# Optimization experiments

Measured on AMD Instinct MI355X. Metric: run time of the kernel, lower is better.

Reference implementation:

```python
import jax, jax.numpy as jnp
import numpy as np

Z, Y, X = 32, 480, 480          # sparse voxel grid (LiDAR-scale)
N = 200_000                     # active voxels
C_IN, C_OUT = 64, 64
EPS = 1e-5


def _subm_conv(f, nbr, w):
    """Submanifold sparse conv as gather-matmul-accumulate.
    f: [N, Cin]; nbr: [N, K] neighbor row ids, pad index == N for missing;
    w: [K, Cin, Cout]."""
    f_pad = jnp.concatenate([f, jnp.zeros((1, f.shape[1]), f.dtype)], axis=0)
    g = f_pad[nbr]                       # [N, K, Cin] gathered neighbor features
    return jnp.einsum('nkc,kco->no', g, w)


def _bn(x, gamma, beta):
    # BatchNorm1d in training mode: batch stats over the N dimension
    m = x.mean(axis=0)
    v = x.var(axis=0)
    return (x - m) * jax.lax.rsqrt(v + EPS) * gamma + beta


def setup_inputs() -> dict:
    rng = np.random.default_rng(0)
    ids = rng.choice(Z * Y * X, size=N, replace=False)
    lookup = np.full(Z * Y * X, -1, dtype=np.int64)
    lookup[ids] = np.arange(N)
    z = ids // (Y * X)
    y = (ids // X) % Y
    x = ids % X

    def nbr_table(offsets):
        cols = []
        for dz, dy, dx in offsets:
            zz, yy, xx = z + dz, y + dy, x + dx
            ok = (zz >= 0) & (zz < Z) & (yy >= 0) & (yy < Y) & (xx >= 0) & (xx < X)
            lin = np.clip((zz * Y + yy) * X + xx, 0, Z * Y * X - 1)
            idx = np.where(ok, lookup[lin], -1)
            cols.append(np.where(idx >= 0, idx, N))   # pad index N -> zero row
        return jnp.asarray(np.stack(cols, axis=1).astype(np.int32))

    off13 = [(0, dy, dx) for dy in (-1, 0, 1) for dx in (-1, 0, 1)]  # kernel (1,3,3)
    off31 = [(dz, 0, dx) for dz in (-1, 0, 1) for dx in (-1, 0, 1)]  # kernel (3,1,3)

    key = jax.random.key(0)
    ks = jax.random.split(key, 5)
    s = 0.05
    ones = jnp.ones((C_OUT,), jnp.float32)
    zeros = jnp.zeros((C_OUT,), jnp.float32)
    return {
        'features': jax.random.normal(ks[0], (N, C_IN), jnp.float32),
        'w1':   jax.random.normal(ks[1], (9, C_IN, C_OUT), jnp.float32) * s,
        'w1_2': jax.random.normal(ks[2], (9, C_OUT, C_OUT), jnp.float32) * s,
        'w2':   jax.random.normal(ks[3], (9, C_IN, C_OUT), jnp.float32) * s,
        'w3':   jax.random.normal(ks[4], (9, C_OUT, C_OUT), jnp.float32) * s,
        'g0': ones, 'b0': zeros, 'g0_2': ones, 'b0_2': zeros,
        'g1': ones, 'b1': zeros, 'g2': ones, 'b2': zeros,
        'nbr13': nbr_table(off13),
        'nbr31': nbr_table(off31),
    }


def reference(features, w1, w1_2, w2, w3, g0, b0, g0_2, b0_2, g1, b1, g2, b2,
              nbr13, nbr31):
    # shortcut branch: conv1x3 -> LeakyReLU -> BN -> conv3x1 -> LeakyReLU -> BN
    sc = _subm_conv(features, nbr13, w1)
    sc = _bn(jax.nn.leaky_relu(sc), g0, b0)
    sc = _subm_conv(sc, nbr31, w1_2)
    sc = _bn(jax.nn.leaky_relu(sc), g0_2, b0_2)
    # main branch: conv3x1 -> LeakyReLU -> BN -> conv1x3 -> LeakyReLU -> BN
    r = _subm_conv(features, nbr31, w2)
    r = _bn(jax.nn.leaky_relu(r), g1, b1)
    r = _subm_conv(r, nbr13, w3)
    r = _bn(jax.nn.leaky_relu(r), g2, b2)
    return r + sc
```

## Files before the change

kernel.cpp:

```cpp
#include <hip/hip_runtime.h>

#define NVOX 200000
#define TM 128
#define NBLK 1563
#define NREP 32
#define STG 4224

typedef unsigned short u16;
typedef unsigned int u32;
typedef __bf16 bf16x8 __attribute__((ext_vector_type(8)));
typedef float f32x16 __attribute__((ext_vector_type(16)));

__device__ __forceinline__ float bf2f(u16 h) { return __uint_as_float(((u32)h) << 16); }
__device__ __forceinline__ u16 f2bf(float x) {
  u32 u = __float_as_uint(x);
  u32 r = u + 0x7fffu + ((u >> 16) & 1u);
  return (u16)(r >> 16);
}
__device__ __forceinline__ uint4 cvt8(uint4 a, uint4 b) {
  const float* fa = (const float*)&a;
  const float* fb = (const float*)&b;
  uint4 r;
  u16* q = (u16*)&r;
#pragma unroll
  for (int j = 0; j < 4; ++j) { q[j] = f2bf(fa[j]); q[4 + j] = f2bf(fb[j]); }
  return r;
}

template <int PHASE>
__global__ __launch_bounds__(256, 4)
void conv_fused(const u16* __restrict__ inA, const u16* __restrict__ inB,
                const int* __restrict__ nbrA, const int* __restrict__ nbrB,
                const u16* __restrict__ wfA, const u16* __restrict__ wfB,
                const u16* __restrict__ zrow,
                void* yA, void* yB, float* __restrict__ stA, float* __restrict__ stB) {
  __shared__ __align__(16) float fb4[64 * 68];
  __shared__ float sred[4][128];

  const int tid = threadIdx.x;
  const int bid = blockIdx.x;
  const bool hB = (bid >= NBLK);
  const int blk = hB ? bid - NBLK : bid;
  const u16* f = hB ? inB : inA;
  const int* nbr = hB ? nbrB : nbrA;
  const u16* wf = hB ? wfB : wfA;
  float* st = hB ? stB : stA;

  const int wv = tid >> 6;
  const int lane = tid & 63;
  const int lrow = lane & 31;
  const int lq = lane >> 5;
  const int base = blk * TM;
  const int gr = base + wv * 32 + lrow;

  int ids[9];
#pragma unroll
  for (int j = 0; j < 9; ++j) ids[j] = (gr < NVOX) ? nbr[gr * 9 + j] : NVOX;

  f32x16 acc0 = {0.f, 0.f, 0.f, 0.f, 0.f, 0.f, 0.f, 0.f,
                 0.f, 0.f, 0.f, 0.f, 0.f, 0.f, 0.f, 0.f};
  f32x16 acc1 = acc0;
  constexpr bool FOLDED = (PHASE == 1);
  constexpr int KSTRIDE = FOLDED ? 5120 : 4096;

  uint4 bufA[4], bufB[4];

  auto lda = [&](uint4 (&d)[4], int k) {
    const u16* p = (ids[k] < NVOX) ? (f + (size_t)ids[k] * 64) : zrow;
    p += lq * 8;
#pragma unroll
    for (int i = 0; i < 4; ++i) d[i] = *(const uint4*)(p + i * 16);
  };

  auto mma = [&](const uint4 (&s)[4], int k) {
    const u16* wb = wf + k * KSTRIDE;
#pragma unroll
    for (int ksi = 0; ksi < 4; ++ksi) {
      bf16x8 a = __builtin_bit_cast(bf16x8, s[ksi]);
      bf16x8 b0 = __builtin_bit_cast(bf16x8, *(const uint4*)(wb + (ksi * 2) * 512 + lane * 8));
      bf16x8 b1 = __builtin_bit_cast(bf16x8, *(const uint4*)(wb + (ksi * 2 + 1) * 512 + lane * 8));
      acc0 = __builtin_amdgcn_mfma_f32_32x32x16_bf16(a, b0, acc0, 0, 0, 0);
      acc1 = __builtin_amdgcn_mfma_f32_32x32x16_bf16(a, b1, acc1, 0, 0, 0);
    }
    if constexpr (FOLDED) {
      uint4 a4 = make_uint4(0u, 0u, 0u, 0u);
      if (lq == 0 && ids[k] < NVOX) ((u16*)&a4)[0] = 0x3F80u;
      bf16x8 a = __builtin_bit_cast(bf16x8, a4);
      bf16x8 b0 = __builtin_bit_cast(bf16x8, *(const uint4*)(wb + 8 * 512 + lane * 8));
      bf16x8 b1 = __builtin_bit_cast(bf16x8, *(const uint4*)(wb + 9 * 512 + lane * 8));
      acc0 = __builtin_amdgcn_mfma_f32_32x32x16_bf16(a, b0, acc0, 0, 0, 0);
      acc1 = __builtin_amdgcn_mfma_f32_32x32x16_bf16(a, b1, acc1, 0, 0, 0);
    }
  };

  lda(bufA, 0); lda(bufB, 1);
  mma(bufA, 0);
  lda(bufA, 2); mma(bufB, 1);
  lda(bufB, 3); mma(bufA, 2);
  lda(bufA, 4); mma(bufB, 3);
  lda(bufB, 5); mma(bufA, 4);
  lda(bufA, 6); mma(bufB, 5);
  lda(bufB, 7); mma(bufA, 6);
  lda(bufA, 8); mma(bufB, 7);
  mma(bufA, 8);

  const int cc0 = lrow, cc1 = 32 + lrow;
  float s0 = 0.f, q0 = 0.f, s1 = 0.f, q1 = 0.f;
  float vout[2][16];
#pragma unroll
  for (int r = 0; r < 16; ++r) {
    float v = acc0[r]; v = v > 0.f ? v : 0.01f * v;
    s0 += v; q0 += v * v; vout[0][r] = v;
    float w = acc1[r]; w = w > 0.f ? w : 0.01f * w;
    s1 += w; q1 += w * w; vout[1][r] = w;
  }
  s0 += __shfl_xor(s0, 32); q0 += __shfl_xor(q0, 32);
  s1 += __shfl_xor(s1, 32); q1 += __shfl_xor(q1, 32);
  if (lq == 0) {
    sred[wv][lrow] = s0; sred[wv][32 + lrow] = s1;
    sred[wv][64 + lrow] = q0; sred[wv][96 + lrow] = q1;
  }

  const bool f32out = (PHASE == 1) && !hB;
  const int trow = tid >> 3, cp = tid & 7;
  u16* bb = (u16*)fb4;
#pragma unroll
  for (int h = 0; h < 2; ++h) {
    __syncthreads();
    if ((wv >> 1) == h) {
      const int lr = 32 * (wv & 1);
#pragma unroll
      for (int r = 0; r < 16; ++r) {
        int rowD = lr + (r & 3) + 8 * (r >> 2) + 4 * lq;
        if (f32out) {
          fb4[rowD * 68 + cc0] = vout[0][r];
          fb4[rowD * 68 + cc1] = vout[1][r];
        } else {
          bb[rowD * 72 + cc0] = f2bf(vout[0][r]);
          bb[rowD * 72 + cc1] = f2bf(vout[1][r]);
        }
      }
    }
    __syncthreads();
    if (f32out) {
      float* y = (float*)yA;
#pragma unroll
      for (int it = 0; it < 2; ++it) {
        int r = it * 32 + trow, row = base + 64 * h + r;
        if (row < NVOX) {
          *(float4*)(y + (size_t)row * 64 + cp * 8) = *(const float4*)(fb4 + r * 68 + cp * 8);
          *(float4*)(y + (size_t)row * 64 + cp * 8 + 4) = *(const float4*)(fb4 + r * 68 + cp * 8 + 4);
        }
      }
    } else {
      u16* y = (u16*)(hB ? yB : yA);
#pragma unroll
      for (int it = 0; it < 2; ++it) {
        int r = it * 32 + trow, row = base + 64 * h + r;
        if (row < NVOX)
          *(uint4*)(y + (size_t)row * 64 + cp * 8) = *(const uint4*)(bb + r * 72 + cp * 8);
      }
    }
  }
  if (tid < 128) {
    int which = tid >> 6, c = tid & 63;
    float v = sred[0][which * 64 + c] + sred[1][which * 64 + c] +
              sred[2][which * 64 + c] + sred[3][which * 64 + c];
    atomicAdd(&st[(bid & (NREP - 1)) * 128 + which * 64 + c], v);
  }
}

template <bool IN_F32, bool FOLDED, int MODE>
__global__ __launch_bounds__(256, 4)
void conv_k(const void* __restrict__ fv, const int* __restrict__ nbr,
            const u16* __restrict__ wf, void* yv, float* __restrict__ st,
            float* io, const float* __restrict__ affD,
            const float* __restrict__ affB) {
  __shared__ __align__(16) float fb[128 * 68];
  __shared__ float sred[4][128];

  const int tid = threadIdx.x;
  const int wv = tid >> 6;
  const int lane = tid & 63;
  const int lrow = lane & 31;
  const int lq = lane >> 5;
  const int base = blockIdx.x * TM;
  const int gr = base + wv * 32 + lrow;

  int ids[9];
#pragma unroll
  for (int j = 0; j < 9; ++j) ids[j] = (gr < NVOX) ? nbr[gr * 9 + j] : NVOX;

  f32x16 acc0 = {0.f, 0.f, 0.f, 0.f, 0.f, 0.f, 0.f, 0.f,
                 0.f, 0.f, 0.f, 0.f, 0.f, 0.f, 0.f, 0.f};
  f32x16 acc1 = acc0;
  constexpr int KSTRIDE = FOLDED ? 5120 : 4096;

#pragma unroll
  for (int k = 0; k < 9; ++k) {
    if (k != 4) {
      if (__ballot(ids[k] < NVOX) == 0ull) continue;
    }
    const int id = ids[k];
    const bool ok = id < NVOX;
    uint4 af[4];
    if constexpr (IN_F32) {
      const float* p = (const float*)fv + (size_t)id * 64 + lq * 8;
#pragma unroll
      for (int ksi = 0; ksi < 4; ++ksi) {
        uint4 v0 = make_uint4(0u, 0u, 0u, 0u), v1 = v0;
        if (ok) { v0 = *(const uint4*)(p + ksi * 16); v1 = *(const uint4*)(p + ksi * 16 + 4); }
        af[ksi] = cvt8(v0, v1);
      }
    } else {
      const u16* p = (const u16*)fv + (size_t)id * 64 + lq * 8;
#pragma unroll
      for (int ksi = 0; ksi < 4; ++ksi) {
        uint4 v = make_uint4(0u, 0u, 0u, 0u);
        if (ok) v = *(const uint4*)(p + ksi * 16);
        af[ksi] = v;
      }
    }
    const u16* wb = wf + k * KSTRIDE;
#pragma unroll
    for (int ksi = 0; ksi < 4; ++ksi) {
      bf16x8 a = __builtin_bit_cast(bf16x8, af[ksi]);
      bf16x8 b0 = __builtin_bit_cast(bf16x8, *(const uint4*)(wb + (ksi * 2) * 512 + lane * 8));
      bf16x8 b1 = __builtin_bit_cast(bf16x8, *(const uint4*)(wb + (ksi * 2 + 1) * 512 + lane * 8));
      acc0 = __builtin_amdgcn_mfma_f32_32x32x16_bf16(a, b0, acc0, 0, 0, 0);
      acc1 = __builtin_amdgcn_mfma_f32_32x32x16_bf16(a, b1, acc1, 0, 0, 0);
    }
    if constexpr (FOLDED) {
      uint4 a4 = make_uint4(0u, 0u, 0u, 0u);
      if (lq == 0 && ok) ((u16*)&a4)[0] = 0x3F80u;
      bf16x8 a = __builtin_bit_cast(bf16x8, a4);
      bf16x8 b0 = __builtin_bit_cast(bf16x8, *(const uint4*)(wb + 8 * 512 + lane * 8));
      bf16x8 b1 = __builtin_bit_cast(bf16x8, *(const uint4*)(wb + 9 * 512 + lane * 8));
      acc0 = __builtin_amdgcn_mfma_f32_32x32x16_bf16(a, b0, acc0, 0, 0, 0);
      acc1 = __builtin_amdgcn_mfma_f32_32x32x16_bf16(a, b1, acc1, 0, 0, 0);
    }
  }

  const int cc0 = lrow, cc1 = 32 + lrow;
  float aD0 = 0.f, aD1 = 0.f, hD0 = 0.f, hD1 = 0.f;
  if constexpr (MODE == 2) {
    aD0 = affD[cc0]; hD0 = affD[64 + cc0];
    aD1 = affD[cc1]; hD1 = affD[64 + cc1];
  }
  float s0 = 0.f, q0 = 0.f, s1 = 0.f, q1 = 0.f;
  float vout[2][16];
#pragma unroll
  for (int r = 0; r < 16; ++r) {
    float v = acc0[r]; v = v > 0.f ? v : 0.01f * v;
    s0 += v; q0 += v * v; vout[0][r] = v;
    float w = acc1[r]; w = w > 0.f ? w : 0.01f * w;
    s1 += w; q1 += w * w; vout[1][r] = w;
  }
  if constexpr (MODE != 2) {
    s0 += __shfl_xor(s0, 32); q0 += __shfl_xor(q0, 32);
    s1 += __shfl_xor(s1, 32); q1 += __shfl_xor(q1, 32);
    if (lq == 0) {
      sred[wv][lrow] = s0; sred[wv][32 + lrow] = s1;
      sred[wv][64 + lrow] = q0; sred[wv][96 + lrow] = q1;
    }
  }
  if constexpr (MODE == 0) {
    u16* bb = (u16*)fb;
#pragma unroll
    for (int r = 0; r < 16; ++r) {
      int rowD = 32 * wv + (r & 3) + 8 * (r >> 2) + 4 * lq;
      bb[rowD * 72 + cc0] = f2bf(vout[0][r]);
      bb[rowD * 72 + cc1] = f2bf(vout[1][r]);
    }
  } else if constexpr (MODE == 2 || MODE == 3) {
#pragma unroll
    for (int r = 0; r < 16; ++r) {
      int rowD = 32 * wv + (r & 3) + 8 * (r >> 2) + 4 * lq;
      float v0 = vout[0][r], v1 = vout[1][r];
      if constexpr (MODE == 2) { v0 = fmaf(v0, aD0, hD0); v1 = fmaf(v1, aD1, hD1); }
      fb[rowD * 68 + cc0] = v0;
      fb[rowD * 68 + cc1] = v1;
    }
  }
  __syncthreads();

  const int trow = tid >> 3, cp = tid & 7;
  if constexpr (MODE == 0) {
    u16* y = (u16*)yv;
    const u16* bb = (const u16*)fb;
#pragma unroll
    for (int it = 0; it < 4; ++it) {
      int r = it * 32 + trow, row = base + r;
      if (row < NVOX)
        *(uint4*)(y + (size_t)row * 64 + cp * 8) = *(const uint4*)(bb + r * 72 + cp * 8);
    }
  }
  if constexpr (MODE == 3) {
    float* y = (float*)yv;
#pragma unroll
    for (int it = 0; it < 4; ++it) {
      int r = it * 32 + trow, row = base + r;
      if (row < NVOX) {
        *(float4*)(y + (size_t)row * 64 + cp * 8) = *(const float4*)(fb + r * 68 + cp * 8);
        *(float4*)(y + (size_t)row * 64 + cp * 8 + 4) = *(const float4*)(fb + r * 68 + cp * 8 + 4);
      }
    }
  }
  if constexpr (MODE == 2) {
    float* y = (float*)yv;
#pragma unroll
    for (int it = 0; it < 4; ++it) {
      int r = it * 32 + trow, row = base + r;
      if (row < NVOX) {
        float t[8], p[8], o[8];
        *(float4*)&t[0] = *(const float4*)(fb + r * 68 + cp * 8);
        *(float4*)&t[4] = *(const float4*)(fb + r * 68 + cp * 8 + 4);
        *(float4*)&p[0] = *(const float4*)(io + (size_t)row * 64 + cp * 8);
        *(float4*)&p[4] = *(const float4*)(io + (size_t)row * 64 + cp * 8 + 4);
#pragma unroll
        for (int j = 0; j < 8; ++j) {
          int c = cp * 8 + j;
          o[j] = t[j] + fmaf(p[j], affB[c], affB[64 + c]);
        }
        *(float4*)(y + (size_t)row * 64 + cp * 8) = *(const float4*)&o[0];
        *(float4*)(y + (size_t)row * 64 + cp * 8 + 4) = *(const float4*)&o[4];
      }
    }
  }
  if constexpr (MODE != 2) {
    if (tid < 128) {
      int which = tid >> 6, c = tid & 63;
      float v = sred[0][which * 64 + c] + sred[1][which * 64 + c] +
                sred[2][which * 64 + c] + sred[3][which * 64 + c];
      atomicAdd(&st[(blockIdx.x & (NREP - 1)) * 128 + which * 64 + c], v);
    }
  }
}

__global__ void prep_all(const float* __restrict__ feat, const float* __restrict__ w1,
                         const float* __restrict__ w2, u16* __restrict__ wf,
                         u16* __restrict__ F, float* __restrict__ st,
                         u16* __restrict__ zr, int cvt_blocks) {
  const int bid = blockIdx.x, tid = threadIdx.x;
  if (bid < cvt_blocks) {
    int i8 = (bid * 256 + tid) * 8;
    if (i8 < NVOX * 64) {
      uint4 a = *(const uint4*)(feat + i8);
      uint4 b = *(const uint4*)(feat + i8 + 4);
      *(uint4*)(F + i8) = cvt8(a, b);
    }
    return;
  }
  int rb = bid - cvt_blocks;
  if (rb < 288) {
    int e = rb * 256 + tid;
    int slot = e / 36864, r = e % 36864;
    int k = r >> 12, rr = r & 4095;
    int frag = rr >> 9, lane = (rr >> 3) & 63, j = rr & 7;
    int ks = frag >> 1, ct = frag & 1;
    int cin = ks * 16 + (lane >> 5) * 8 + j;
    int cout = ct * 32 + (lane & 31);
    const float* src = slot ? w2 : w1;
    wf[e] = f2bf(src[k * 4096 + cin * 64 + cout]);
    return;
  }
  for (int i = tid; i < 4 * STG; i += 256) st[i] = 0.f;
  if (tid < 32) ((u32*)zr)[tid] = 0u;
}

__device__ __forceinline__ void bn_from_replicas(const float* stp, const float* g,
                                                 const float* b, int c,
                                                 float* sc, float* sh) {
  float s = 0.f, q = 0.f;
#pragma unroll
  for (int r = 0; r < NREP; ++r) {
    s += stp[r * 128 + c];
    q += stp[r * 128 + 64 + c];
  }
  const float invn = 1.0f / (float)NVOX;
  float mean = s * invn;
  float var = q * invn - mean * mean;
  float sca = g[c] * rsqrtf(var + 1e-5f);
  *sc = sca;
  *sh = b[c] - mean * sca;
}

__global__ void wscale2(const float* __restrict__ wA, float* __restrict__ stpA,
                        const float* __restrict__ gA, const float* __restrict__ bA,
                        u16* __restrict__ dA,
                        const float* __restrict__ wB, float* __restrict__ stpB,
                        const float* __restrict__ gB, const float* __restrict__ bB,
                        u16* __restrict__ dB) {
  __shared__ float sc[64], sh[64];
  const int tid = threadIdx.x;
  const bool hB = (blockIdx.x >= 180);
  const float* wraw = hB ? wB : wA;
  float* stp = hB ? stpB : stpA;
  const float* g = hB ? gB : gA;
  const float* b = hB ? bB : bA;
  u16* dst = hB ? dB : dA;
  const int blk = hB ? blockIdx.x - 180 : blockIdx.x;
  if (tid < 64) {
    float a, h;
    bn_from_replicas(stp, g, b, tid, &a, &h);
    sc[tid] = a; sh[tid] = h;
    if (blk == 0) { stp[NREP * 128 + tid] = a; stp[NREP * 128 + 64 + tid] = h; }
  }
  __syncthreads();
  int e = blk * 256 + tid;
  int k = e / 5120, r = e % 5120;
  int frag = r >> 9, lane = (r >> 3) & 63, j = r & 7;
  int ks = frag >> 1, ct = frag & 1;
  int cout = ct * 32 + (lane & 31);
  u16 val = 0;
  if (ks < 4) {
    int cin = ks * 16 + (lane >> 5) * 8 + j;
    val = f2bf(sc[cin] * wraw[k * 4096 + cin * 64 + cout]);
  } else if (((lane >> 5) == 0) && j == 0) {
    float acc = 0.f;
    for (int c = 0; c < 64; ++c) acc += sh[c] * wraw[k * 4096 + c * 64 + cout];
    val = f2bf(acc);
  }
  dst[e] = val;
}

__global__ void finalize2(float* __restrict__ stA, const float* __restrict__ gA,
                          const float* __restrict__ bA, float* __restrict__ stB,
                          const float* __restrict__ gB, const float* __restrict__ bB) {
  int t = threadIdx.x;
  float* stp = (t < 64) ? stA : stB;
  const float* g = (t < 64) ? gA : gB;
  const float* b = (t < 64) ? bA : bB;
  int c = t & 63;
  if (t < 128) {
    float a, h;
    bn_from_replicas(stp, g, b, c, &a, &h);
    stp[NREP * 128 + c] = a;
    stp[NREP * 128 + 64 + c] = h;
  }
}

__global__ void final_add(const u16* __restrict__ y3, float* io,
                          const float* __restrict__ affB, const float* __restrict__ affD) {
  int i8 = (blockIdx.x * 256 + threadIdx.x) * 8;
  if (i8 < NVOX * 64) {
    float a[8];
    *(float4*)&a[0] = *(const float4*)(io + i8);
    *(float4*)&a[4] = *(const float4*)(io + i8 + 4);
    uint4 vd = *(const uint4*)(y3 + i8);
    const u16* pd = (const u16*)&vd;
    int cb = i8 & 63;
    float o[8];
#pragma unroll
    for (int j = 0; j < 8; ++j) {
      int c = cb + j;
      o[j] = fmaf(a[j], affB[c], affB[64 + c]) + fmaf(bf2f(pd[j]), affD[c], affD[64 + c]);
    }
    *(float4*)(io + i8) = *(const float4*)&o[0];
    *(float4*)(io + i8 + 4) = *(const float4*)&o[4];
  }
}

extern "C" void kernel_launch(void* const* d_in, const int* in_sizes, int n_in,
                              void* d_out, int out_size, void* d_ws, size_t ws_size,
                              hipStream_t stream) {
  const float* feat = (const float*)d_in[0];
  const float* w1 = (const float*)d_in[1];
  const float* w1_2 = (const float*)d_in[2];
  const float* w2 = (const float*)d_in[3];
  const float* w3 = (const float*)d_in[4];
  const float* g0 = (const float*)d_in[5];
  const float* b0 = (const float*)d_in[6];
  const float* g0_2 = (const float*)d_in[7];
  const float* b0_2 = (const float*)d_in[8];
  const float* g1 = (const float*)d_in[9];
  const float* b1 = (const float*)d_in[10];
  const float* g2 = (const float*)d_in[11];
  const float* b2 = (const float*)d_in[12];
  const int* nbr13 = (const int*)d_in[13];
  const int* nbr31 = (const int*)d_in[14];
  float* out = (float*)d_out;

  char* ws = (char*)d_ws;
  float* st = (float*)ws;
  u16* wf = (u16*)(ws + 67584);
  u16* s0 = wf;
  u16* s1 = wf + 36864;
  u16* s2 = wf + 73728;
  u16* s3 = wf + 119808;
  u16* zr = (u16*)(ws + 399360);
  u16* F = (u16*)(ws + 399488);
  u16* A1 = F + (size_t)NVOX * 64;
  u16* A2 = A1 + (size_t)NVOX * 64;
  const size_t base_sz = 399488;
  const size_t need_fused = base_sz + 3ull * NVOX * 64 * 2;
  const size_t need_serial = base_sz + 2ull * NVOX * 64 * 2;

  float* st0 = st, *st1 = st + STG, *st2 = st + 2 * STG, *st3 = st + 3 * STG;

  if (ws_size >= need_fused) {
    prep_all<<<6539, 256, 0, stream>>>(feat, w1, w2, wf, F, st, zr, 6250);
    conv_fused<0><<<2 * NBLK, 256, 0, stream>>>(F, F, nbr13, nbr31, s0, s1, zr,
                                                A1, A2, st0, st2);
    wscale2<<<360, 256, 0, stream>>>(w1_2, st0, g0, b0, s2, w3, st2, g1, b1, s3);
    conv_fused<1><<<2 * NBLK, 256, 0, stream>>>(A1, A2, nbr31, nbr13, s2, s3, zr,
                                                out, F, st1, st3);
    finalize2<<<1, 128, 0, stream>>>(st1, g0_2, b0_2, st3, g2, b2);
    final_add<<<6250, 256, 0, stream>>>(F, out, st1 + NREP * 128, st3 + NREP * 128);
  } else if (ws_size >= need_serial) {
    prep_all<<<6539, 256, 0, stream>>>(feat, w1, w2, wf, F, st, zr, 6250);
    conv_k<false, false, 0><<<NBLK, 256, 0, stream>>>(F, nbr13, s0, A1, st0, nullptr, nullptr, nullptr);
    wscale2<<<180, 256, 0, stream>>>(w1_2, st0, g0, b0, s2, w3, st2, g1, b1, s3);
    conv_k<false, true, 3><<<NBLK, 256, 0, stream>>>(A1, nbr31, s2, out, st1, nullptr, nullptr, nullptr);
    conv_k<false, false, 0><<<NBLK, 256, 0, stream>>>(F, nbr31, s1, A1, st2, nullptr, nullptr, nullptr);
    wscale2<<<360, 256, 0, stream>>>(w1_2, st0, g0, b0, s2, w3, st2, g1, b1, s3);
    conv_k<false, true, 0><<<NBLK, 256, 0, stream>>>(A1, nbr13, s3, F, st3, nullptr, nullptr, nullptr);
    finalize2<<<1, 128, 0, stream>>>(st1, g0_2, b0_2, st3, g2, b2);
    final_add<<<6250, 256, 0, stream>>>(F, out, st1 + NREP * 128, st3 + NREP * 128);
  } else {
    u16* Az = F;
    prep_all<<<289, 256, 0, stream>>>(feat, w1, w2, wf, nullptr, st, zr, 0);
    conv_k<true, false, 0><<<NBLK, 256, 0, stream>>>(feat, nbr13, s0, Az, st0, nullptr, nullptr, nullptr);
    wscale2<<<180, 256, 0, stream>>>(w1_2, st0, g0, b0, s2, w3, st2, g1, b1, s3);
    conv_k<false, true, 3><<<NBLK, 256, 0, stream>>>(Az, nbr31, s2, out, st1, nullptr, nullptr, nullptr);
    finalize2<<<1, 128, 0, stream>>>(st1, g0_2, b0_2, st3, g2, b2);
    conv_k<true, false, 0><<<NBLK, 256, 0, stream>>>(feat, nbr31, s1, Az, st2, nullptr, nullptr, nullptr);
    wscale2<<<360, 256, 0, stream>>>(w1_2, st0, g0, b0, s2, w3, st2, g1, b1, s3);
    conv_k<false, true, 1><<<NBLK, 256, 0, stream>>>(Az, nbr13, s3, nullptr, st3, nullptr, nullptr, nullptr);
    finalize2<<<1, 128, 0, stream>>>(st1, g0_2, b0_2, st3, g2, b2);
    conv_k<false, true, 2><<<NBLK, 256, 0, stream>>>(Az, nbr13, s3, out, nullptr, out,
                                                     st3 + NREP * 128, st1 + NREP * 128);
  }
}
```

Measured before the change: 286.5 us.

## Process three row groups per wave with register-held weights and skip empty neighbors

Each wave now handles 96 rows in three 32-row groups, so every per-offset weight fragment is loaded into registers once and reused across three row groups. Neighbor ids are prefetched one offset ahead, and gathers plus MFMAs are skipped when no lane in a group has a valid neighbor for that offset. The LDS-staged coalesced store epilogue is replaced by direct scattered per-element global stores, and the grid shrinks to a third with launch bounds lowered to 2 blocks per SM. The aim is to cut repeated weight loads and wasted gather/MMA work, at the cost of higher register pressure, lower occupancy and uncoalesced output writes.

```diff
diff --git a/kernel.cpp b/kernel.cpp
--- a/kernel.cpp
+++ b/kernel.cpp
@@ -3,6 +3,7 @@
 #define NVOX 200000
 #define TM 128
 #define NBLK 1563
+#define NBLK3 521
 #define NREP 32
 #define STG 4224
 
@@ -28,19 +29,18 @@
 }
 
 template <int PHASE>
-__global__ __launch_bounds__(256, 4)
+__global__ __launch_bounds__(256, 2)
 void conv_fused(const u16* __restrict__ inA, const u16* __restrict__ inB,
                 const int* __restrict__ nbrA, const int* __restrict__ nbrB,
                 const u16* __restrict__ wfA, const u16* __restrict__ wfB,
                 const u16* __restrict__ zrow,
                 void* yA, void* yB, float* __restrict__ stA, float* __restrict__ stB) {
-  __shared__ __align__(16) float fb4[64 * 68];
   __shared__ float sred[4][128];
 
   const int tid = threadIdx.x;
   const int bid = blockIdx.x;
-  const bool hB = (bid >= NBLK);
-  const int blk = hB ? bid - NBLK : bid;
+  const bool hB = (bid >= NBLK3);
+  const int blk = hB ? bid - NBLK3 : bid;
   const u16* f = hB ? inB : inA;
   const int* nbr = hB ? nbrB : nbrA;
   const u16* wf = hB ? wfB : wfA;
@@ -50,118 +50,113 @@
   const int lane = tid & 63;
   const int lrow = lane & 31;
   const int lq = lane >> 5;
-  const int base = blk * TM;
-  const int gr = base + wv * 32 + lrow;
-
-  int ids[9];
-#pragma unroll
-  for (int j = 0; j < 9; ++j) ids[j] = (gr < NVOX) ? nbr[gr * 9 + j] : NVOX;
-
-  f32x16 acc0 = {0.f, 0.f, 0.f, 0.f, 0.f, 0.f, 0.f, 0.f,
-                 0.f, 0.f, 0.f, 0.f, 0.f, 0.f, 0.f, 0.f};
-  f32x16 acc1 = acc0;
+  const int wbase = blk * 384 + wv * 96;
+  const int gr0 = wbase + lrow;
+  const int gr1 = gr0 + 32;
+  const int gr2 = gr0 + 64;
+
   constexpr bool FOLDED = (PHASE == 1);
   constexpr int KSTRIDE = FOLDED ? 5120 : 4096;
 
-  uint4 bufA[4], bufB[4];
-
-  auto lda = [&](uint4 (&d)[4], int k) {
-    const u16* p = (ids[k] < NVOX) ? (f + (size_t)ids[k] * 64) : zrow;
-    p += lq * 8;
-#pragma unroll
-    for (int i = 0; i < 4; ++i) d[i] = *(const uint4*)(p + i * 16);
+  f32x16 zz = {0.f, 0.f, 0.f, 0.f, 0.f, 0.f, 0.f, 0.f,
+               0.f, 0.f, 0.f, 0.f, 0.f, 0.f, 0.f, 0.f};
+  f32x16 a00 = zz, a01 = zz, a10 = zz, a11 = zz, a20 = zz, a21 = zz;
+
+  int ic0 = (gr0 < NVOX) ? nbr[gr0 * 9] : NVOX;
+  int ic1 = (gr1 < NVOX) ? nbr[gr1 * 9] : NVOX;
+  int ic2 = (gr2 < NVOX) ? nbr[gr2 * 9] : NVOX;
+
+  uint4 X[4], Y[4];
+
+  for (int k = 0; k < 9; ++k) {
+    const u16* wb = wf + k * KSTRIDE;
+    bf16x8 wreg[8];
+#pragma unroll
+    for (int fi = 0; fi < 8; ++fi)
+      wreg[fi] = __builtin_bit_cast(bf16x8, *(const uint4*)(wb + fi * 512 + lane * 8));
+    bf16x8 wrb0, wrb1;
+    if constexpr (FOLDED) {
+      wrb0 = __builtin_bit_cast(bf16x8, *(const uint4*)(wb + 8 * 512 + lane * 8));
+      wrb1 = __builtin_bit_cast(bf16x8, *(const uint4*)(wb + 9 * 512 + lane * 8));
+    }
+    int in0 = NVOX, in1 = NVOX, in2 = NVOX;
+    if (k < 8) {
+      in0 = (gr0 < NVOX) ? nbr[gr0 * 9 + k + 1] : NVOX;
+      in1 = (gr1 < NVOX) ? nbr[gr1 * 9 + k + 1] : NVOX;
+      in2 = (gr2 < NVOX) ? nbr[gr2 * 9 + k + 1] : NVOX;
+    }
+
+    const bool l0 = (k == 4) || (__ballot(ic0 < NVOX) != 0ull);
+    const bool l1 = (k == 4) || (__ballot(ic1 < NVOX) != 0ull);
+    const bool l2 = (k == 4) || (__ballot(ic2 < NVOX) != 0ull);
+
+    auto G = [&](uint4 (&d)[4], int id) {
+      const u16* p = (id < NVOX) ? (f + (size_t)id * 64) : zrow;
+      p += lq * 8;
+      d[0] = *(const uint4*)(p);
+      d[1] = *(const uint4*)(p + 16);
+      d[2] = *(const uint4*)(p + 32);
+      d[3] = *(const uint4*)(p + 48);
+    };
+    auto MMA = [&](f32x16& c0, f32x16& c1, const uint4 (&s)[4], int id) {
+#pragma unroll
+      for (int ksi = 0; ksi < 4; ++ksi) {
+        bf16x8 a = __builtin_bit_cast(bf16x8, s[ksi]);
+        c0 = __builtin_amdgcn_mfma_f32_32x32x16_bf16(a, wreg[ksi * 2], c0, 0, 0, 0);
+        c1 = __builtin_amdgcn_mfma_f32_32x32x16_bf16(a, wreg[ksi * 2 + 1], c1, 0, 0, 0);
+      }
+      if constexpr (FOLDED) {
+        uint4 a4 = make_uint4(0u, 0u, 0u, 0u);
+        if (lq == 0 && id < NVOX) ((u16*)&a4)[0] = 0x3F80u;
+        bf16x8 a = __builtin_bit_cast(bf16x8, a4);
+        c0 = __builtin_amdgcn_mfma_f32_32x32x16_bf16(a, wrb0, c0, 0, 0, 0);
+        c1 = __builtin_amdgcn_mfma_f32_32x32x16_bf16(a, wrb1, c1, 0, 0, 0);
+      }
+    };
+
+    if (l0) G(X, ic0);
+    if (l1) G(Y, ic1);
+    if (l0) MMA(a00, a01, X, ic0);
+    if (l2) G(X, ic2);
+    if (l1) MMA(a10, a11, Y, ic1);
+    if (l2) MMA(a20, a21, X, ic2);
+
+    ic0 = in0; ic1 = in1; ic2 = in2;
+  }
+
+  const bool f32out = (PHASE == 1) && !hB;
+  float* yf = (float*)yA;
+  u16* yb = (u16*)(hB ? yB : yA);
+  float s0 = 0.f, q0 = 0.f, s1 = 0.f, q1 = 0.f;
+
+  auto EPI = [&](const f32x16& c0, const f32x16& c1, int g) {
+    const int row0 = wbase + g * 32 + 4 * lq;
+#pragma unroll
+    for (int r = 0; r < 16; ++r) {
+      float v = c0[r]; v = v > 0.f ? v : 0.01f * v;
+      float w = c1[r]; w = w > 0.f ? w : 0.01f * w;
+      s0 += v; q0 += v * v; s1 += w; q1 += w * w;
+      const int row = row0 + (r & 3) + 8 * (r >> 2);
+      if (row < NVOX) {
+        if (f32out) {
+          yf[(size_t)row * 64 + lrow] = v;
+          yf[(size_t)row * 64 + 32 + lrow] = w;
+        } else {
+          yb[(size_t)row * 64 + lrow] = f2bf(v);
+          yb[(size_t)row * 64 + 32 + lrow] = f2bf(w);
+        }
+      }
+    }
   };
-
-  auto mma = [&](const uint4 (&s)[4], int k) {
-    const u16* wb = wf + k * KSTRIDE;
-#pragma unroll
-    for (int ksi = 0; ksi < 4; ++ksi) {
-      bf16x8 a = __builtin_bit_cast(bf16x8, s[ksi]);
-      bf16x8 b0 = __builtin_bit_cast(bf16x8, *(const uint4*)(wb + (ksi * 2) * 512 + lane * 8));
-      bf16x8 b1 = __builtin_bit_cast(bf16x8, *(const uint4*)(wb + (ksi * 2 + 1) * 512 + lane * 8));
-      acc0 = __builtin_amdgcn_mfma_f32_32x32x16_bf16(a, b0, acc0, 0, 0, 0);
-      acc1 = __builtin_amdgcn_mfma_f32_32x32x16_bf16(a, b1, acc1, 0, 0, 0);
-    }
-    if constexpr (FOLDED) {
-      uint4 a4 = make_uint4(0u, 0u, 0u, 0u);
-      if (lq == 0 && ids[k] < NVOX) ((u16*)&a4)[0] = 0x3F80u;
-      bf16x8 a = __builtin_bit_cast(bf16x8, a4);
-      bf16x8 b0 = __builtin_bit_cast(bf16x8, *(const uint4*)(wb + 8 * 512 + lane * 8));
-      bf16x8 b1 = __builtin_bit_cast(bf16x8, *(const uint4*)(wb + 9 * 512 + lane * 8));
-      acc0 = __builtin_amdgcn_mfma_f32_32x32x16_bf16(a, b0, acc0, 0, 0, 0);
-      acc1 = __builtin_amdgcn_mfma_f32_32x32x16_bf16(a, b1, acc1, 0, 0, 0);
-    }
-  };
-
-  lda(bufA, 0); lda(bufB, 1);
-  mma(bufA, 0);
-  lda(bufA, 2); mma(bufB, 1);
-  lda(bufB, 3); mma(bufA, 2);
-  lda(bufA, 4); mma(bufB, 3);
-  lda(bufB, 5); mma(bufA, 4);
-  lda(bufA, 6); mma(bufB, 5);
-  lda(bufB, 7); mma(bufA, 6);
-  lda(bufA, 8); mma(bufB, 7);
-  mma(bufA, 8);
-
-  const int cc0 = lrow, cc1 = 32 + lrow;
-  float s0 = 0.f, q0 = 0.f, s1 = 0.f, q1 = 0.f;
-  float vout[2][16];
-#pragma unroll
-  for (int r = 0; r < 16; ++r) {
-    float v = acc0[r]; v = v > 0.f ? v : 0.01f * v;
-    s0 += v; q0 += v * v; vout[0][r] = v;
-    float w = acc1[r]; w = w > 0.f ? w : 0.01f * w;
-    s1 += w; q1 += w * w; vout[1][r] = w;
-  }
+  EPI(a00, a01, 0); EPI(a10, a11, 1); EPI(a20, a21, 2);
+
   s0 += __shfl_xor(s0, 32); q0 += __shfl_xor(q0, 32);
   s1 += __shfl_xor(s1, 32); q1 += __shfl_xor(q1, 32);
   if (lq == 0) {
     sred[wv][lrow] = s0; sred[wv][32 + lrow] = s1;
     sred[wv][64 + lrow] = q0; sred[wv][96 + lrow] = q1;
   }
-
-  const bool f32out = (PHASE == 1) && !hB;
-  const int trow = tid >> 3, cp = tid & 7;
-  u16* bb = (u16*)fb4;
-#pragma unroll
-  for (int h = 0; h < 2; ++h) {
-    __syncthreads();
-    if ((wv >> 1) == h) {
-      const int lr = 32 * (wv & 1);
-#pragma unroll
-      for (int r = 0; r < 16; ++r) {
-        int rowD = lr + (r & 3) + 8 * (r >> 2) + 4 * lq;
-        if (f32out) {
-          fb4[rowD * 68 + cc0] = vout[0][r];
-          fb4[rowD * 68 + cc1] = vout[1][r];
-        } else {
-          bb[rowD * 72 + cc0] = f2bf(vout[0][r]);
-          bb[rowD * 72 + cc1] = f2bf(vout[1][r]);
-        }
-      }
-    }
-    __syncthreads();
-    if (f32out) {
-      float* y = (float*)yA;
-#pragma unroll
-      for (int it = 0; it < 2; ++it) {
-        int r = it * 32 + trow, row = base + 64 * h + r;
-        if (row < NVOX) {
-          *(float4*)(y + (size_t)row * 64 + cp * 8) = *(const float4*)(fb4 + r * 68 + cp * 8);
-          *(float4*)(y + (size_t)row * 64 + cp * 8 + 4) = *(const float4*)(fb4 + r * 68 + cp * 8 + 4);
-        }
-      }
-    } else {
-      u16* y = (u16*)(hB ? yB : yA);
-#pragma unroll
-      for (int it = 0; it < 2; ++it) {
-        int r = it * 32 + trow, row = base + 64 * h + r;
-        if (row < NVOX)
-          *(uint4*)(y + (size_t)row * 64 + cp * 8) = *(const uint4*)(bb + r * 72 + cp * 8);
-      }
-    }
-  }
+  __syncthreads();
   if (tid < 128) {
     int which = tid >> 6, c = tid & 63;
     float v = sred[0][which * 64 + c] + sred[1][which * 64 + c] +
@@ -500,11 +495,11 @@
 
   if (ws_size >= need_fused) {
     prep_all<<<6539, 256, 0, stream>>>(feat, w1, w2, wf, F, st, zr, 6250);
-    conv_fused<0><<<2 * NBLK, 256, 0, stream>>>(F, F, nbr13, nbr31, s0, s1, zr,
-                                                A1, A2, st0, st2);
+    conv_fused<0><<<2 * NBLK3, 256, 0, stream>>>(F, F, nbr13, nbr31, s0, s1, zr,
+                                                 A1, A2, st0, st2);
     wscale2<<<360, 256, 0, stream>>>(w1_2, st0, g0, b0, s2, w3, st2, g1, b1, s3);
-    conv_fused<1><<<2 * NBLK, 256, 0, stream>>>(A1, A2, nbr31, nbr13, s2, s3, zr,
-                                                out, F, st1, st3);
+    conv_fused<1><<<2 * NBLK3, 256, 0, stream>>>(A1, A2, nbr31, nbr13, s2, s3, zr,
+                                                 out, F, st1, st3);
     finalize2<<<1, 128, 0, stream>>>(st1, g0_2, b0_2, st3, g2, b2);
     final_add<<<6250, 256, 0, stream>>>(F, out, st1 + NREP * 128, st3 + NREP * 128);
   } else if (ws_size >= need_serial) {
```

Result: faster. 271.1 us (-5.4%).

## Skip wave-empty neighbor offsets in gather-MMA and fuse BN finalize into final add

Applied to the files above, without the earlier changes.

The conv kernel now takes a wave-wide ballot for each of the 9 kernel offsets and runs the gather and MFMA only for offsets that at least one of the wave's 32 rows actually has. The center offset is always kept. This targets the large share of empty neighbors in a sparse grid (about 200k of 7.4M voxels are active). It also folds the single-block finalize2 launch into the final add kernel, so each block recomputes the BN affine from the replica stats. In exchange, the loop becomes data-dependent and loses its static software pipelining, and the BN reduction is repeated in every block.

```diff
diff --git a/kernel.cpp b/kernel.cpp
--- a/kernel.cpp
+++ b/kernel.cpp
@@ -25,6 +25,9 @@
 #pragma unroll
   for (int j = 0; j < 4; ++j) { q[j] = f2bf(fa[j]); q[4 + j] = f2bf(fb[j]); }
   return r;
+}
+__device__ __forceinline__ int popnext(u32& m) {
+  int k = __builtin_ctz(m); m &= m - 1; return k;
 }
 
 template <int PHASE>
@@ -52,27 +55,36 @@
   const int lq = lane >> 5;
   const int base = blk * TM;
   const int gr = base + wv * 32 + lrow;
-
-  int ids[9];
-#pragma unroll
-  for (int j = 0; j < 9; ++j) ids[j] = (gr < NVOX) ? nbr[gr * 9 + j] : NVOX;
+  const bool okrow = (gr < NVOX);
+  const int* nrow = nbr + (size_t)(okrow ? gr : 0) * 9;
+
+  constexpr bool FOLDED = (PHASE == 1);
+  constexpr int KSTRIDE = FOLDED ? 5120 : 4096;
+
+  u32 live = 1u << 4;
+  {
+    int idt[9];
+#pragma unroll
+    for (int j = 0; j < 9; ++j) idt[j] = okrow ? nrow[j] : NVOX;
+#pragma unroll
+    for (int j = 0; j < 9; ++j)
+      if (j != 4 && __ballot(idt[j] < NVOX) != 0ull) live |= 1u << j;
+  }
 
   f32x16 acc0 = {0.f, 0.f, 0.f, 0.f, 0.f, 0.f, 0.f, 0.f,
                  0.f, 0.f, 0.f, 0.f, 0.f, 0.f, 0.f, 0.f};
   f32x16 acc1 = acc0;
-  constexpr bool FOLDED = (PHASE == 1);
-  constexpr int KSTRIDE = FOLDED ? 5120 : 4096;
-
-  uint4 bufA[4], bufB[4];
-
-  auto lda = [&](uint4 (&d)[4], int k) {
-    const u16* p = (ids[k] < NVOX) ? (f + (size_t)ids[k] * 64) : zrow;
+
+  auto LDID = [&](int k) { return okrow ? nrow[k] : NVOX; };
+  auto G = [&](uint4 (&d)[4], int id) {
+    const u16* p = (id < NVOX) ? (f + (size_t)id * 64) : zrow;
     p += lq * 8;
-#pragma unroll
-    for (int i = 0; i < 4; ++i) d[i] = *(const uint4*)(p + i * 16);
+    d[0] = *(const uint4*)(p);
+    d[1] = *(const uint4*)(p + 16);
+    d[2] = *(const uint4*)(p + 32);
+    d[3] = *(const uint4*)(p + 48);
   };
-
-  auto mma = [&](const uint4 (&s)[4], int k) {
+  auto MMA = [&](const uint4 (&s)[4], int k, int id) {
     const u16* wb = wf + k * KSTRIDE;
 #pragma unroll
     for (int ksi = 0; ksi < 4; ++ksi) {
@@ -84,7 +96,7 @@
     }
     if constexpr (FOLDED) {
       uint4 a4 = make_uint4(0u, 0u, 0u, 0u);
-      if (lq == 0 && ids[k] < NVOX) ((u16*)&a4)[0] = 0x3F80u;
+      if (lq == 0 && id < NVOX) ((u16*)&a4)[0] = 0x3F80u;
       bf16x8 a = __builtin_bit_cast(bf16x8, a4);
       bf16x8 b0 = __builtin_bit_cast(bf16x8, *(const uint4*)(wb + 8 * 512 + lane * 8));
       bf16x8 b1 = __builtin_bit_cast(bf16x8, *(const uint4*)(wb + 9 * 512 + lane * 8));
@@ -93,16 +105,23 @@
     }
   };
 
-  lda(bufA, 0); lda(bufB, 1);
-  mma(bufA, 0);
-  lda(bufA, 2); mma(bufB, 1);
-  lda(bufB, 3); mma(bufA, 2);
-  lda(bufA, 4); mma(bufB, 3);
-  lda(bufB, 5); mma(bufA, 4);
-  lda(bufA, 6); mma(bufB, 5);
-  lda(bufB, 7); mma(bufA, 6);
-  lda(bufA, 8); mma(bufB, 7);
-  mma(bufA, 8);
+  {
+    uint4 X[4], Y[4];
+    int k0 = popnext(live);
+    int id0 = LDID(k0);
+    G(X, id0);
+    while (true) {
+      int k1 = -1, id1 = NVOX;
+      if (live) { k1 = popnext(live); id1 = LDID(k1); G(Y, id1); }
+      MMA(X, k0, id0);
+      if (k1 < 0) break;
+      int k2 = -1, id2 = NVOX;
+      if (live) { k2 = popnext(live); id2 = LDID(k2); G(X, id2); }
+      MMA(Y, k1, id1);
+      if (k2 < 0) break;
+      k0 = k2; id0 = id2;
+    }
+  }
 
   const int cc0 = lrow, cc1 = 32 + lrow;
   float s0 = 0.f, q0 = 0.f, s1 = 0.f, q1 = 0.f;
@@ -461,6 +480,38 @@
   }
 }
 
+__global__ void final_add2(const u16* __restrict__ y3, float* io,
+                           float* __restrict__ stB, const float* __restrict__ gB,
+                           const float* __restrict__ bB,
+                           float* __restrict__ stD, const float* __restrict__ gD,
+                           const float* __restrict__ bD) {
+  __shared__ float aff[4][64];
+  const int t = threadIdx.x;
+  if (t < 128) {
+    float a, h;
+    if (t < 64) { bn_from_replicas(stB, gB, bB, t, &a, &h); aff[0][t] = a; aff[1][t] = h; }
+    else { int c = t - 64; bn_from_replicas(stD, gD, bD, c, &a, &h); aff[2][c] = a; aff[3][c] = h; }
+  }
+  __syncthreads();
+  int i8 = (blockIdx.x * 256 + t) * 8;
+  if (i8 < NVOX * 64) {
+    float a[8];
+    *(float4*)&a[0] = *(const float4*)(io + i8);
+    *(float4*)&a[4] = *(const float4*)(io + i8 + 4);
+    uint4 vd = *(const uint4*)(y3 + i8);
+    const u16* pd = (const u16*)&vd;
+    int cb = i8 & 63;
+    float o[8];
+#pragma unroll
+    for (int j = 0; j < 8; ++j) {
+      int c = cb + j;
+      o[j] = fmaf(a[j], aff[0][c], aff[1][c]) + fmaf(bf2f(pd[j]), aff[2][c], aff[3][c]);
+    }
+    *(float4*)(io + i8) = *(const float4*)&o[0];
+    *(float4*)(io + i8 + 4) = *(const float4*)&o[4];
+  }
+}
+
 extern "C" void kernel_launch(void* const* d_in, const int* in_sizes, int n_in,
                               void* d_out, int out_size, void* d_ws, size_t ws_size,
                               hipStream_t stream) {
@@ -505,8 +556,7 @@
     wscale2<<<360, 256, 0, stream>>>(w1_2, st0, g0, b0, s2, w3, st2, g1, b1, s3);
     conv_fused<1><<<2 * NBLK, 256, 0, stream>>>(A1, A2, nbr31, nbr13, s2, s3, zr,
                                                 out, F, st1, st3);
-    finalize2<<<1, 128, 0, stream>>>(st1, g0_2, b0_2, st3, g2, b2);
-    final_add<<<6250, 256, 0, stream>>>(F, out, st1 + NREP * 128, st3 + NREP * 128);
+    final_add2<<<6250, 256, 0, stream>>>(F, out, st1, g0_2, b0_2, st3, g2, b2);
   } else if (ws_size >= need_serial) {
     prep_all<<<6539, 256, 0, stream>>>(feat, w1, w2, wf, F, st, zr, 6250);
     conv_k<false, false, 0><<<NBLK, 256, 0, stream>>>(F, nbr13, s0, A1, st0, nullptr, nullptr, nullptr);
```

New measurement: 280.2 us. 2.2% less time.
